# Kernel tuning notes

Hardware: AMD Instinct MI355X
Metric: run time of the kernel (lower is better)

## Reference

```python
import jax, jax.numpy as jnp
import numpy as np

HID = 16

def _mean_agg(feat, src, dst, n):
    # scatter-mean of source features into destination nodes (PyG aggr='mean')
    s = jax.ops.segment_sum(feat[src], dst, num_segments=n)
    deg = jax.ops.segment_sum(jnp.ones((src.shape[0], 1), feat.dtype), dst, num_segments=n)
    return s / jnp.maximum(deg, 1.0)


def setup_inputs() -> dict:
    key = jax.random.key(0)
    ks = jax.random.split(key, 12)
    N, E, F = 100000, 1600000, 64
    x = jax.random.normal(ks[0], (N, F), dtype=jnp.float32)
    edge_index = jax.random.randint(ks[1], (2, E), 0, N, dtype=jnp.int64)
    edge_weight = jnp.zeros((E,), dtype=jnp.int64)  # edge_type, relation 0 everywhere
    h_0 = jax.random.normal(ks[2], (N, HID), dtype=jnp.float32)
    c_0 = jax.random.normal(ks[3], (N, HID), dtype=jnp.float32)
    # stacked RGCNConv params for gates (i, f, c, o):
    #   Wx/Rx act on x (in=F), Wh/Rh act on h (in=HID); W=message weight, R=root weight
    sx = 1.0 / np.sqrt(F)
    sh = 1.0 / np.sqrt(HID)
    Wx = jax.random.normal(ks[4], (4, F, HID), dtype=jnp.float32) * sx
    Rx = jax.random.normal(ks[5], (4, F, HID), dtype=jnp.float32) * sx
    bx = jnp.zeros((4, HID), dtype=jnp.float32)
    Wh = jax.random.normal(ks[6], (4, HID, HID), dtype=jnp.float32) * sh
    Rh = jax.random.normal(ks[7], (4, HID, HID), dtype=jnp.float32) * sh
    bh = jnp.zeros((4, HID), dtype=jnp.float32)
    lin_w = jax.random.normal(ks[8], (HID, 1), dtype=jnp.float32) * sh
    lin_b = jnp.zeros((1,), dtype=jnp.float32)
    return {"x": x, "edge_index": edge_index, "edge_weight": edge_weight,
            "h_0": h_0, "c_0": c_0, "Wx": Wx, "Rx": Rx, "bx": bx,
            "Wh": Wh, "Rh": Rh, "bh": bh, "lin_w": lin_w, "lin_b": lin_b}


def reference(x, edge_index, edge_weight, h_0, c_0, Wx, Rx, bx, Wh, Rh, bh, lin_w, lin_b):
    # edge_weight is used by LRGCN as edge_type; with num_relations=1 it is all
    # zeros and every edge belongs to relation 0, so it drops out of the math.
    n = x.shape[0]
    src, dst = edge_index[0], edge_index[1]
    agg_x = _mean_agg(x, src, dst, n)    # [N, F]  shared across all 4 gates
    agg_h = _mean_agg(h_0, src, dst, n)  # [N, HID]
    # gate pre-activations: conv_x_g(x) + conv_h_g(h), g in {i,f,c,o}
    pre = (jnp.einsum('nd,gdo->gno', agg_x, Wx) + jnp.einsum('nd,gdo->gno', x, Rx)
           + bx[:, None, :]
           + jnp.einsum('nd,gdo->gno', agg_h, Wh) + jnp.einsum('nd,gdo->gno', h_0, Rh)
           + bh[:, None, :])  # [4, N, HID]
    i_g = jax.nn.sigmoid(pre[0])
    f_g = jax.nn.sigmoid(pre[1])
    t_g = jnp.tanh(pre[2])
    o_g = jax.nn.sigmoid(pre[3])
    c_new = f_g * c_0 + i_g * t_g
    h_new = o_g * jnp.tanh(c_new)
    out = jax.nn.relu(h_new) @ lin_w + lin_b  # [N, 1]
    return out, h_new, c_new
```

## Files before the change

kernel.cpp:

```cpp
#include <hip/hip_runtime.h>


#define F_IN 64
#define NHID 16
#define BSH  6
#define NPB  64
#define SEGW 512
#define PARTB (SEGW / 2)
#define EMAX 1280

__device__ __forceinline__ unsigned pack_bf16x2(float lo, float hi) {
    unsigned a = __float_as_uint(lo);
    unsigned b = __float_as_uint(hi);
    a = (a + 0x7fffu + ((a >> 16) & 1u)) >> 16;
    b = (b + 0x7fffu + ((b >> 16) & 1u)) >> 16;
    return a | (b << 16);
}
__device__ __forceinline__ float fast_sigmoid(float v) {
    return 1.f / (1.f + __expf(-v));
}
__device__ __forceinline__ float fast_tanh(float v) {
    return 1.f - 2.f / (1.f + __expf(2.f * v));
}
__device__ __forceinline__ void fma4(float4& a, float s, const float4& wv) {
    a.x += s * wv.x; a.y += s * wv.y; a.z += s * wv.z; a.w += s * wv.w;
}

__global__ __launch_bounds__(128) void fused_pp2(
        const int* __restrict__ ei, uint2* __restrict__ pairs,
        int* __restrict__ cnts, int E, int epw, int nbkt, int nbktp,
        const float* __restrict__ x, const float* __restrict__ h0,
        const float* __restrict__ Wx, const float* __restrict__ Wh,
        const float* __restrict__ Rx, const float* __restrict__ Rh,
        const float* __restrict__ bx, const float* __restrict__ bh,
        unsigned* __restrict__ mxb, unsigned* __restrict__ rootb,
        int n, int partBlocks) {
    extern __shared__ char smem[];
    int tid = threadIdx.x;

    if ((int)blockIdx.x < partBlocks) {
        int* cnt_s = (int*)smem;
        int wv = tid >> 6, lane = tid & 63;
        int seg = blockIdx.x * 2 + wv;
        int* cnt = cnt_s + wv * nbktp;

        for (int i = lane; i < nbktp; i += 64) cnt[i] = 0;
        __syncthreads();

        int beg = seg * epw;
        int end = beg + epw; if (end > E) end = E;

        for (int e = beg + lane; e < end; e += 64)
            atomicAdd(&cnt[((unsigned)ei[E + e]) >> BSH], 1);
        __syncthreads();

        int per = (nbkt + 63) >> 6;
        int s0 = lane * per;
        int s1 = s0 + per; if (s1 > nbkt) s1 = nbkt;
        if (s0 > nbkt) s0 = nbkt;
        int sum = 0;
        for (int i = s0; i < s1; ++i) sum += cnt[i];
        int inc = sum;
#pragma unroll
        for (int off = 1; off < 64; off <<= 1) {
            int v = __shfl_up(inc, off);
            if (lane >= off) inc += v;
        }
        int run = inc - sum;
        for (int i = s0; i < s1; ++i) { int c = cnt[i]; cnt[i] = run; run += c; }
        if (lane == 63) cnt[nbkt] = run;
        __syncthreads();

        for (int i = lane; i <= nbkt; i += 64)
            cnts[(size_t)seg * nbktp + i] = cnt[i];

        uint2* wreg = pairs + (size_t)seg * epw;
        for (int e = beg + lane; e < end; e += 64) {
            unsigned s = (unsigned)ei[e];
            unsigned d = (unsigned)ei[E + e];
            int pos = atomicAdd(&cnt[d >> BSH], 1);
            wreg[pos] = make_uint2(s, d);
        }
        return;
    }

    float* sx = (float*)smem;
    float* sh = sx + 32 * 68;
    int nodeBase = ((int)blockIdx.x - partBlocks) * 32;

#pragma unroll
    for (int i = 0; i < 4; ++i) {
        int idx = i * 128 + tid;
        int row = idx >> 4, c4 = idx & 15;
        int node = nodeBase + row;
        float4 v = make_float4(0.f, 0.f, 0.f, 0.f);
        if (node < n) v = ((const float4*)(x + (size_t)node * F_IN))[c4];
        *(float4*)(sx + row * 68 + c4 * 4) = v;
    }
    {
        int row = tid >> 2, c4 = tid & 3;
        int node = nodeBase + row;
        float4 v = make_float4(0.f, 0.f, 0.f, 0.f);
        if (node < n) v = ((const float4*)(h0 + (size_t)node * NHID))[c4];
        *(float4*)(sh + row * 20 + c4 * 4) = v;
    }
    __syncthreads();

    int grp = tid >> 4, q = tid & 15;
    int g = q >> 2, rr = q & 3;
    const float* wxp = Wx + g * (F_IN * NHID) + rr * 4;
    const float* rxp = Rx + g * (F_IN * NHID) + rr * 4;
    const float* whp = Wh + g * (NHID * NHID) + rr * 4;
    const float* rhp = Rh + g * (NHID * NHID) + rr * 4;
    const float* sx0 = sx + (grp * 4 + 0) * 68;
    const float* sx1 = sx + (grp * 4 + 1) * 68;
    const float* sx2 = sx + (grp * 4 + 2) * 68;
    const float* sx3 = sx + (grp * 4 + 3) * 68;
    const float* sh0 = sh + (grp * 4 + 0) * 20;
    const float* sh1 = sh + (grp * 4 + 1) * 20;
    const float* sh2 = sh + (grp * 4 + 2) * 20;
    const float* sh3 = sh + (grp * 4 + 3) * 20;

    float4 m0 = make_float4(0.f, 0.f, 0.f, 0.f), m1 = m0, m2 = m0, m3 = m0;
    float4 r0 = m0, r1 = m0, r2 = m0, r3 = m0;

    float4 w0 = *(const float4*)(wxp + 0 * NHID);
    float4 w1 = *(const float4*)(wxp + 1 * NHID);
    float4 w2 = *(const float4*)(wxp + 2 * NHID);
    float4 w3 = *(const float4*)(wxp + 3 * NHID);
    float4 v0 = *(const float4*)(rxp + 0 * NHID);
    float4 v1 = *(const float4*)(rxp + 1 * NHID);
    float4 v2 = *(const float4*)(rxp + 2 * NHID);
    float4 v3 = *(const float4*)(rxp + 3 * NHID);
#pragma unroll 1
    for (int k = 0; k < F_IN; k += 4) {
        float4 xa = *(const float4*)(sx0 + k);
        float4 xb = *(const float4*)(sx1 + k);
        float4 xc = *(const float4*)(sx2 + k);
        float4 xd = *(const float4*)(sx3 + k);
        int kn = (k + 4 < F_IN) ? k + 4 : 0;
        float4 t0 = *(const float4*)(wxp + (kn + 0) * NHID);
        float4 t1 = *(const float4*)(wxp + (kn + 1) * NHID);
        float4 t2 = *(const float4*)(wxp + (kn + 2) * NHID);
        float4 t3 = *(const float4*)(wxp + (kn + 3) * NHID);
        float4 u0 = *(const float4*)(rxp + (kn + 0) * NHID);
        float4 u1 = *(const float4*)(rxp + (kn + 1) * NHID);
        float4 u2 = *(const float4*)(rxp + (kn + 2) * NHID);
        float4 u3 = *(const float4*)(rxp + (kn + 3) * NHID);
        fma4(m0, xa.x, w0); fma4(m0, xa.y, w1); fma4(m0, xa.z, w2); fma4(m0, xa.w, w3);
        fma4(m1, xb.x, w0); fma4(m1, xb.y, w1); fma4(m1, xb.z, w2); fma4(m1, xb.w, w3);
        fma4(m2, xc.x, w0); fma4(m2, xc.y, w1); fma4(m2, xc.z, w2); fma4(m2, xc.w, w3);
        fma4(m3, xd.x, w0); fma4(m3, xd.y, w1); fma4(m3, xd.z, w2); fma4(m3, xd.w, w3);
        fma4(r0, xa.x, v0); fma4(r0, xa.y, v1); fma4(r0, xa.z, v2); fma4(r0, xa.w, v3);
        fma4(r1, xb.x, v0); fma4(r1, xb.y, v1); fma4(r1, xb.z, v2); fma4(r1, xb.w, v3);
        fma4(r2, xc.x, v0); fma4(r2, xc.y, v1); fma4(r2, xc.z, v2); fma4(r2, xc.w, v3);
        fma4(r3, xd.x, v0); fma4(r3, xd.y, v1); fma4(r3, xd.z, v2); fma4(r3, xd.w, v3);
        w0 = t0; w1 = t1; w2 = t2; w3 = t3;
        v0 = u0; v1 = u1; v2 = u2; v3 = u3;
    }
    w0 = *(const float4*)(whp + 0 * NHID);
    w1 = *(const float4*)(whp + 1 * NHID);
    w2 = *(const float4*)(whp + 2 * NHID);
    w3 = *(const float4*)(whp + 3 * NHID);
    v0 = *(const float4*)(rhp + 0 * NHID);
    v1 = *(const float4*)(rhp + 1 * NHID);
    v2 = *(const float4*)(rhp + 2 * NHID);
    v3 = *(const float4*)(rhp + 3 * NHID);
#pragma unroll 1
    for (int k = 0; k < NHID; k += 4) {
        float4 xa = *(const float4*)(sh0 + k);
        float4 xb = *(const float4*)(sh1 + k);
        float4 xc = *(const float4*)(sh2 + k);
        float4 xd = *(const float4*)(sh3 + k);
        int kn = (k + 4 < NHID) ? k + 4 : 0;
        float4 t0 = *(const float4*)(whp + (kn + 0) * NHID);
        float4 t1 = *(const float4*)(whp + (kn + 1) * NHID);
        float4 t2 = *(const float4*)(whp + (kn + 2) * NHID);
        float4 t3 = *(const float4*)(whp + (kn + 3) * NHID);
        float4 u0 = *(const float4*)(rhp + (kn + 0) * NHID);
        float4 u1 = *(const float4*)(rhp + (kn + 1) * NHID);
        float4 u2 = *(const float4*)(rhp + (kn + 2) * NHID);
        float4 u3 = *(const float4*)(rhp + (kn + 3) * NHID);
        fma4(m0, xa.x, w0); fma4(m0, xa.y, w1); fma4(m0, xa.z, w2); fma4(m0, xa.w, w3);
        fma4(m1, xb.x, w0); fma4(m1, xb.y, w1); fma4(m1, xb.z, w2); fma4(m1, xb.w, w3);
        fma4(m2, xc.x, w0); fma4(m2, xc.y, w1); fma4(m2, xc.z, w2); fma4(m2, xc.w, w3);
        fma4(m3, xd.x, w0); fma4(m3, xd.y, w1); fma4(m3, xd.z, w2); fma4(m3, xd.w, w3);
        fma4(r0, xa.x, v0); fma4(r0, xa.y, v1); fma4(r0, xa.z, v2); fma4(r0, xa.w, v3);
        fma4(r1, xb.x, v0); fma4(r1, xb.y, v1); fma4(r1, xb.z, v2); fma4(r1, xb.w, v3);
        fma4(r2, xc.x, v0); fma4(r2, xc.y, v1); fma4(r2, xc.z, v2); fma4(r2, xc.w, v3);
        fma4(r3, xd.x, v0); fma4(r3, xd.y, v1); fma4(r3, xd.z, v2); fma4(r3, xd.w, v3);
        w0 = t0; w1 = t1; w2 = t2; w3 = t3;
        v0 = u0; v1 = u1; v2 = u2; v3 = u3;
    }
    {
        float4 b1 = *(const float4*)(bx + q * 4);
        float4 b2 = *(const float4*)(bh + q * 4);
        float bxx = b1.x + b2.x, byy = b1.y + b2.y;
        float bzz = b1.z + b2.z, bww = b1.w + b2.w;
        r0.x += bxx; r0.y += byy; r0.z += bzz; r0.w += bww;
        r1.x += bxx; r1.y += byy; r1.z += bzz; r1.w += bww;
        r2.x += bxx; r2.y += byy; r2.z += bzz; r2.w += bww;
        r3.x += bxx; r3.y += byy; r3.z += bzz; r3.w += bww;
    }

    __syncthreads();
    *(float4*)(sx + (grp * 4 + 0) * 68 + q * 4) = m0;
    *(float4*)(sx + (grp * 4 + 1) * 68 + q * 4) = m1;
    *(float4*)(sx + (grp * 4 + 2) * 68 + q * 4) = m2;
    *(float4*)(sx + (grp * 4 + 3) * 68 + q * 4) = m3;
    __syncthreads();
#pragma unroll
    for (int i = 0; i < 4; ++i) {
        int node = nodeBase + grp * 4 + i;
        if (node < n) {
            const float* rowp = sx + (grp * 4 + i) * 68;
            float a0 = rowp[q], a1 = rowp[16 + q], a2 = rowp[32 + q], a3 = rowp[48 + q];
            ((uint2*)(mxb + (size_t)node * 32))[q] =
                make_uint2(pack_bf16x2(a0, a1), pack_bf16x2(a2, a3));
        }
    }
    if (rootb != nullptr) {
        __syncthreads();
        *(float4*)(sx + (grp * 4 + 0) * 68 + q * 4) = r0;
        *(float4*)(sx + (grp * 4 + 1) * 68 + q * 4) = r1;
        *(float4*)(sx + (grp * 4 + 2) * 68 + q * 4) = r2;
        *(float4*)(sx + (grp * 4 + 3) * 68 + q * 4) = r3;
        __syncthreads();
#pragma unroll
        for (int i = 0; i < 4; ++i) {
            int node = nodeBase + grp * 4 + i;
            if (node < n) {
                const float* rowp = sx + (grp * 4 + i) * 68;
                float a0 = rowp[q], a1 = rowp[16 + q], a2 = rowp[32 + q], a3 = rowp[48 + q];
                ((uint2*)(rootb + (size_t)node * 32))[q] =
                    make_uint2(pack_bf16x2(a0, a1), pack_bf16x2(a2, a3));
            }
        }
    }
}

__global__ __launch_bounds__(256) void hub_kernel(
        const float* __restrict__ c0, const float* __restrict__ lin_w,
        const float* __restrict__ lin_b,
        const unsigned* __restrict__ mxb, const unsigned* __restrict__ rootb,
        const uint2* __restrict__ pairs, const int* __restrict__ cnts,
        float* __restrict__ out, int n, int epw, int nbktp) {
    __shared__ int deg[NPB], rowptr[NPB], cursor[NPB];
    __shared__ unsigned stage[EMAX];
    __shared__ int csr[EMAX];
    __shared__ int scnt;
    int tid = threadIdx.x;

    int nb = gridDim.x;
    int qq = nb >> 3, rr2 = nb & 7;
    int xcd = blockIdx.x & 7, ix = blockIdx.x >> 3;
    int b = (xcd < rr2) ? xcd * (qq + 1) + ix
                        : rr2 * (qq + 1) + (xcd - rr2) * qq + ix;
    int nstart = b << BSH;

    if (tid < NPB) deg[tid] = 0;
    if (tid == 0) scnt = 0;
    __syncthreads();

    int seg0 = tid, seg1 = tid + 256;
    const int* cr0 = cnts + (size_t)seg0 * nbktp;
    const int* cr1 = cnts + (size_t)seg1 * nbktp;
    int o1a = cr0[b], o2a = cr0[b + 1];
    int o1b = cr1[b], o2b = cr1[b + 1];
    int tot = (o2a - o1a) + (o2b - o1b);
    int idx = 0;
    if (tot > 0) idx = atomicAdd(&scnt, tot);
    {
        const uint2* p = pairs + (size_t)seg0 * epw;
        for (int i = o1a; i < o2a; ++i, ++idx) {
            uint2 pr = p[i];
            if (idx < EMAX) {
                int dl = (int)pr.y - nstart;
                stage[idx] = pr.x | ((unsigned)dl << 26);
                atomicAdd(&deg[dl], 1);
            }
        }
        p = pairs + (size_t)seg1 * epw;
        for (int i = o1b; i < o2b; ++i, ++idx) {
            uint2 pr = p[i];
            if (idx < EMAX) {
                int dl = (int)pr.y - nstart;
                stage[idx] = pr.x | ((unsigned)dl << 26);
                atomicAdd(&deg[dl], 1);
            }
        }
    }
    __syncthreads();

    if (tid < 64) {
        int lane = tid;
        int v = deg[lane];
        int inc = v;
#pragma unroll
        for (int off = 1; off < 64; off <<= 1) {
            int t = __shfl_up(inc, off);
            if (lane >= off) inc += t;
        }
        rowptr[lane] = inc - v;
        cursor[lane] = inc - v;
    }
    __syncthreads();

    int sc = scnt < EMAX ? scnt : EMAX;
    for (int i = tid; i < sc; i += 256) {
        unsigned v = stage[i];
        int dl = v >> 26;
        int pos = atomicAdd(&cursor[dl], 1);
        csr[pos] = (int)(v & 0x03FFFFFFu);
    }
    __syncthreads();

    int grp = tid >> 4, q = tid & 15;
    for (int ln = grp; ln < NPB; ln += 16) {
        int node = nstart + ln;
        if (node >= n) continue;
        int cnt = deg[ln];
        const int* row = &csr[rowptr[ln]];

        float ax = 0.f, ay = 0.f, az = 0.f, aw = 0.f;
        int base = 0;
        for (; base + 16 <= cnt; base += 16) {
            int eid = row[base + q];
#pragma unroll
            for (int k = 0; k < 16; ++k) {
                int s = __shfl(eid, k, 16);
                uint2 v = *((const uint2*)(mxb + (size_t)s * 32) + q);
                ax += __uint_as_float(v.x << 16);
                ay += __uint_as_float(v.x & 0xffff0000u);
                az += __uint_as_float(v.y << 16);
                aw += __uint_as_float(v.y & 0xffff0000u);
            }
        }
        int m = cnt - base;
        if (m > 0) {
            int eid = (q < m) ? row[base + q] : 0;
            for (int k = 0; k < m; ++k) {
                int s = __shfl(eid, k, 16);
                uint2 v = *((const uint2*)(mxb + (size_t)s * 32) + q);
                ax += __uint_as_float(v.x << 16);
                ay += __uint_as_float(v.x & 0xffff0000u);
                az += __uint_as_float(v.y << 16);
                aw += __uint_as_float(v.y & 0xffff0000u);
            }
        }

        uint2 rv = *((const uint2*)(rootb + (size_t)node * 32) + q);
        float inv = 1.f / fmaxf((float)cnt, 1.f);
        float px = ax * inv + __uint_as_float(rv.x << 16);
        float py = ay * inv + __uint_as_float(rv.x & 0xffff0000u);
        float pz = az * inv + __uint_as_float(rv.y << 16);
        float pw = aw * inv + __uint_as_float(rv.y & 0xffff0000u);

        float ig = fast_sigmoid(px);
        float fg = fast_sigmoid(py);
        float tg = fast_tanh(pz);
        float og = fast_sigmoid(pw);

        float cn = fg * c0[(size_t)node * NHID + q] + ig * tg;
        float hn = og * fast_tanh(cn);

        out[(size_t)n + (size_t)node * NHID + q] = hn;
        out[(size_t)n + (size_t)n * NHID + (size_t)node * NHID + q] = cn;

        float p = fmaxf(hn, 0.f) * lin_w[q];
#pragma unroll
        for (int off = 8; off; off >>= 1) p += __shfl_xor(p, off, 16);
        if (q == 0) out[node] = p + lin_b[0];
    }
}

__global__ void zero_int_kernel(int4* __restrict__ p, int n4) {
    int i = blockIdx.x * blockDim.x + threadIdx.x;
    if (i < n4) p[i] = make_int4(0, 0, 0, 0);
}
__global__ void scatter_direct_kernel(const int* __restrict__ ei,
                                      int* __restrict__ cursor,
                                      int* __restrict__ csrp, int E, int cap) {
    int e = blockIdx.x * blockDim.x + threadIdx.x;
    if (e < E) {
        int d = ei[E + e];
        int pos = atomicAdd(&cursor[d], 1);
        if (pos < cap) csrp[(size_t)d * cap + pos] = ei[e];
    }
}
__global__ __launch_bounds__(256) void gfinal_inl(
        const float* __restrict__ x, const float* __restrict__ h0,
        const float* __restrict__ c0,
        const float* __restrict__ Rx, const float* __restrict__ Rh,
        const float* __restrict__ bx, const float* __restrict__ bh,
        const float* __restrict__ lin_w, const float* __restrict__ lin_b,
        const unsigned* __restrict__ mxb, const int* __restrict__ csrp,
        const int* __restrict__ cursor,
        float* __restrict__ out, int n, int cap) {
    __shared__ float sm[16 * 68];
    int idx = blockIdx.x * 256 + threadIdx.x;
    int node = idx >> 4, q = idx & 15;
    int nl = threadIdx.x >> 4;
    bool valid = node < n;

    int cnt = 0;
    if (valid) cnt = cursor[node];
    int mt = cnt < cap ? cnt : cap;
    const int* row = csrp + (size_t)node * cap;

    float ax = 0.f, ay = 0.f, az = 0.f, aw = 0.f;
    int base = 0;
    for (; base + 16 <= mt; base += 16) {
        int eid = row[base + q];
#pragma unroll
        for (int k = 0; k < 16; ++k) {
            int s = __shfl(eid, k, 16);
            uint2 v = *((const uint2*)(mxb + (size_t)s * 32) + q);
            ax += __uint_as_float(v.x << 16);
            ay += __uint_as_float(v.x & 0xffff0000u);
            az += __uint_as_float(v.y << 16);
            aw += __uint_as_float(v.y & 0xffff0000u);
        }
    }
    int mrem = mt - base;
    if (mrem > 0) {
        int eid = (q < mrem) ? row[base + q] : 0;
        for (int k = 0; k < mrem; ++k) {
            int s = __shfl(eid, k, 16);
            uint2 v = *((const uint2*)(mxb + (size_t)s * 32) + q);
            ax += __uint_as_float(v.x << 16);
            ay += __uint_as_float(v.x & 0xffff0000u);
            az += __uint_as_float(v.y << 16);
            aw += __uint_as_float(v.y & 0xffff0000u);
        }
    }

    float4 r = make_float4(0.f, 0.f, 0.f, 0.f);
    if (valid) {
        int g = q >> 2, rr = q & 3;
        const float* xr = x + (size_t)node * F_IN;
        const float* hr = h0 + (size_t)node * NHID;
        const float* rx = Rx + g * (F_IN * NHID) + rr * 4;
        const float* rh = Rh + g * (NHID * NHID) + rr * 4;
#pragma unroll 8
        for (int k = 0; k < F_IN; ++k) fma4(r, xr[k], *(const float4*)(rx + k * NHID));
#pragma unroll
        for (int k = 0; k < NHID; ++k) fma4(r, hr[k], *(const float4*)(rh + k * NHID));
        float4 b1 = *(const float4*)(bx + q * 4);
        float4 b2 = *(const float4*)(bh + q * 4);
        r.x += b1.x + b2.x; r.y += b1.y + b2.y;
        r.z += b1.z + b2.z; r.w += b1.w + b2.w;
    }
    *(float4*)(sm + nl * 68 + q * 4) = r;
    __syncthreads();

    if (valid) {
        const float* rowp = sm + nl * 68;
        float inv = 1.f / fmaxf((float)cnt, 1.f);
        float px = ax * inv + rowp[q];
        float py = ay * inv + rowp[16 + q];
        float pz = az * inv + rowp[32 + q];
        float pw = aw * inv + rowp[48 + q];
        float ig = fast_sigmoid(px);
        float fg = fast_sigmoid(py);
        float tg = fast_tanh(pz);
        float og = fast_sigmoid(pw);
        float cn = fg * c0[(size_t)node * NHID + q] + ig * tg;
        float hn = og * fast_tanh(cn);
        out[(size_t)n + (size_t)node * NHID + q] = hn;
        out[(size_t)n + (size_t)n * NHID + (size_t)node * NHID + q] = cn;
        float p = fmaxf(hn, 0.f) * lin_w[q];
#pragma unroll
        for (int off = 8; off; off >>= 1) p += __shfl_xor(p, off, 16);
        if (q == 0) out[node] = p + lin_b[0];
    }
}

extern "C" void kernel_launch(void* const* d_in, const int* in_sizes, int n_in,
                              void* d_out, int out_size, void* d_ws, size_t ws_size,
                              hipStream_t stream) {
    const float* x     = (const float*)d_in[0];
    const int*   ei    = (const int*)d_in[1];
    const float* h0    = (const float*)d_in[3];
    const float* c0    = (const float*)d_in[4];
    const float* Wx    = (const float*)d_in[5];
    const float* Rx    = (const float*)d_in[6];
    const float* bx    = (const float*)d_in[7];
    const float* Wh    = (const float*)d_in[8];
    const float* Rh    = (const float*)d_in[9];
    const float* bh    = (const float*)d_in[10];
    const float* lin_w = (const float*)d_in[11];
    const float* lin_b = (const float*)d_in[12];

    const int N = in_sizes[3] / NHID;
    const int E = in_sizes[1] / 2;
    const int NBKT  = (N + NPB - 1) >> BSH;
    const int nbktp = ((NBKT + 1) + 15) & ~15;
    const int epw   = ((E + SEGW - 1) / SEGW + 7) & ~7;

    const size_t mxb_u   = (size_t)N * 32;
    const size_t root_u  = (size_t)N * 32;
    const size_t pairs_u = 2ull * SEGW * epw;
    const size_t cnts_u  = (size_t)SEGW * nbktp;
    const size_t need = (mxb_u + root_u + pairs_u + cnts_u) * 4;

    unsigned* wsu = (unsigned*)d_ws;
    float* out = (float*)d_out;
    const int projBlocks = (N + 31) / 32;

    size_t ldsPart = (size_t)2 * nbktp * sizeof(int);
    size_t ldsProj = (32 * 68 + 32 * 20) * sizeof(float);
    size_t ldsFused = ldsPart > ldsProj ? ldsPart : ldsProj;

    if (ws_size >= need) {
        unsigned* mxb   = wsu;
        unsigned* rootb = mxb + mxb_u;
        uint2*    pairs = (uint2*)(rootb + root_u);
        int*      cnts  = (int*)(pairs + (size_t)SEGW * epw);

        fused_pp2<<<PARTB + projBlocks, 128, (int)ldsFused, stream>>>(
            ei, pairs, cnts, E, epw, NBKT, nbktp,
            x, h0, Wx, Wh, Rx, Rh, bx, bh, mxb, rootb, N, PARTB);
        hub_kernel<<<NBKT, 256, 0, stream>>>(
            c0, lin_w, lin_b, mxb, rootb, pairs, cnts, out, N, epw, nbktp);
    } else {
        const int cap = 32;
        const int P = (N + 3) & ~3;
        unsigned* mxb   = wsu;
        int*      cursor= (int*)(mxb + mxb_u);
        int*      csrp  = cursor + P;

        zero_int_kernel<<<(P / 4 + 255) / 256, 256, 0, stream>>>((int4*)cursor, P / 4);
        fused_pp2<<<projBlocks, 128, (int)ldsProj, stream>>>(
            ei, nullptr, nullptr, E, epw, NBKT, nbktp,
            x, h0, Wx, Wh, Rx, Rh, bx, bh, mxb, nullptr, N, 0);
        scatter_direct_kernel<<<(E + 255) / 256, 256, 0, stream>>>(
            ei, cursor, csrp, E, cap);
        gfinal_inl<<<(N * 16 + 255) / 256, 256, 0, stream>>>(
            x, h0, c0, Rx, Rh, bx, bh, lin_w, lin_b, mxb, csrp, cursor,
            out, N, cap);
    }
}
```

Before: 140.3 us.

## Stage gate weights in LDS and double block size of fused partition/projection kernel

Block size of fused_pp2 doubles to 256 threads. Partition blocks now cover four segments each and projection blocks cover 64 nodes each. All Wx/Rx/Wh/Rh weights are copied into padded LDS once per block, and the matmul loops read them from LDS instead of prefetching from global memory through registers. The goal is to cut repeated global/L1 weight traffic and register pressure from software prefetch, at the cost of roughly 64KB of LDS per block, which may limit occupancy. The code not shown after the projection matmul must still handle the 64-node tile correctly.

```diff
diff --git a/kernel.cpp b/kernel.cpp
--- a/kernel.cpp
+++ b/kernel.cpp
@@ -6,8 +6,16 @@
 #define BSH  6
 #define NPB  64
 #define SEGW 512
-#define PARTB (SEGW / 2)
+#define PARTB (SEGW / 4)
 #define EMAX 1280
+
+#define LWX 0
+#define LRX 4128
+#define LWH 8256
+#define LRH 9312
+#define LSX 10368
+#define LSH 14720
+#define LDSF 16000
 
 __device__ __forceinline__ unsigned pack_bf16x2(float lo, float hi) {
     unsigned a = __float_as_uint(lo);
@@ -26,7 +34,7 @@
     a.x += s * wv.x; a.y += s * wv.y; a.z += s * wv.z; a.w += s * wv.w;
 }
 
-__global__ __launch_bounds__(128) void fused_pp2(
+__global__ __launch_bounds__(256) void fused_pp2(
         const int* __restrict__ ei, uint2* __restrict__ pairs,
         int* __restrict__ cnts, int E, int epw, int nbkt, int nbktp,
         const float* __restrict__ x, const float* __restrict__ h0,
@@ -35,13 +43,13 @@
         const float* __restrict__ bx, const float* __restrict__ bh,
         unsigned* __restrict__ mxb, unsigned* __restrict__ rootb,
         int n, int partBlocks) {
-    extern __shared__ char smem[];
+    extern __shared__ float smem[];
     int tid = threadIdx.x;
 
     if ((int)blockIdx.x < partBlocks) {
         int* cnt_s = (int*)smem;
         int wv = tid >> 6, lane = tid & 63;
-        int seg = blockIdx.x * 2 + wv;
+        int seg = blockIdx.x * 4 + wv;
         int* cnt = cnt_s + wv * nbktp;
 
         for (int i = lane; i < nbktp; i += 64) cnt[i] = 0;
@@ -84,13 +92,32 @@
         return;
     }
 
-    float* sx = (float*)smem;
-    float* sh = sx + 32 * 68;
-    int nodeBase = ((int)blockIdx.x - partBlocks) * 32;
+    float* lwx = smem + LWX;
+    float* lrx = smem + LRX;
+    float* lwh = smem + LWH;
+    float* lrh = smem + LRH;
+    float* sx  = smem + LSX;
+    float* sh  = smem + LSH;
+    int nodeBase = ((int)blockIdx.x - partBlocks) * 64;
 
 #pragma unroll
     for (int i = 0; i < 4; ++i) {
-        int idx = i * 128 + tid;
+        int idx = i * 256 + tid;
+        int gg = idx >> 8;
+        int off = (idx & 255) * 4;
+        *(float4*)(lwx + gg * 1032 + off) = ((const float4*)Wx)[idx];
+        *(float4*)(lrx + gg * 1032 + off) = ((const float4*)Rx)[idx];
+    }
+    {
+        int idx = tid;
+        int gg = idx >> 6;
+        int off = (idx & 63) * 4;
+        *(float4*)(lwh + gg * 264 + off) = ((const float4*)Wh)[idx];
+        *(float4*)(lrh + gg * 264 + off) = ((const float4*)Rh)[idx];
+    }
+#pragma unroll
+    for (int i = 0; i < 4; ++i) {
+        int idx = i * 256 + tid;
         int row = idx >> 4, c4 = idx & 15;
         int node = nodeBase + row;
         float4 v = make_float4(0.f, 0.f, 0.f, 0.f);
@@ -108,10 +135,10 @@
 
     int grp = tid >> 4, q = tid & 15;
     int g = q >> 2, rr = q & 3;
-    const float* wxp = Wx + g * (F_IN * NHID) + rr * 4;
-    const float* rxp = Rx + g * (F_IN * NHID) + rr * 4;
-    const float* whp = Wh + g * (NHID * NHID) + rr * 4;
-    const float* rhp = Rh + g * (NHID * NHID) + rr * 4;
+    const float* wxp = lwx + g * 1032 + rr * 4;
+    const float* rxp = lrx + g * 1032 + rr * 4;
+    const float* whp = lwh + g * 264 + rr * 4;
+    const float* rhp = lrh + g * 264 + rr * 4;
     const float* sx0 = sx + (grp * 4 + 0) * 68;
     const float* sx1 = sx + (grp * 4 + 1) * 68;
     const float* sx2 = sx + (grp * 4 + 2) * 68;
@@ -124,29 +151,20 @@
     float4 m0 = make_float4(0.f, 0.f, 0.f, 0.f), m1 = m0, m2 = m0, m3 = m0;
     float4 r0 = m0, r1 = m0, r2 = m0, r3 = m0;
 
-    float4 w0 = *(const float4*)(wxp + 0 * NHID);
-    float4 w1 = *(const float4*)(wxp + 1 * NHID);
-    float4 w2 = *(const float4*)(wxp + 2 * NHID);
-    float4 w3 = *(const float4*)(wxp + 3 * NHID);
-    float4 v0 = *(const float4*)(rxp + 0 * NHID);
-    float4 v1 = *(const float4*)(rxp + 1 * NHID);
-    float4 v2 = *(const float4*)(rxp + 2 * NHID);
-    float4 v3 = *(const float4*)(rxp + 3 * NHID);
 #pragma unroll 1
     for (int k = 0; k < F_IN; k += 4) {
         float4 xa = *(const float4*)(sx0 + k);
         float4 xb = *(const float4*)(sx1 + k);
         float4 xc = *(const float4*)(sx2 + k);
         float4 xd = *(const float4*)(sx3 + k);
-        int kn = (k + 4 < F_IN) ? k + 4 : 0;
-        float4 t0 = *(const float4*)(wxp + (kn + 0) * NHID);
-        float4 t1 = *(const float4*)(wxp + (kn + 1) * NHID);
-        float4 t2 = *(const float4*)(wxp + (kn + 2) * NHID);
-        float4 t3 = *(const float4*)(wxp + (kn + 3) * NHID);
-        float4 u0 = *(const float4*)(rxp + (kn + 0) * NHID);
-        float4 u1 = *(const float4*)(rxp + (kn + 1) * NHID);
-        float4 u2 = *(const float4*)(rxp + (kn + 2) * NHID);
-        float4 u3 = *(const float4*)(rxp + (kn + 3) * NHID);
+        float4 w0 = *(const float4*)(wxp + (k + 0) * NHID);
+        float4 w1 = *(const float4*)(wxp + (k + 1) * NHID);
+        float4 w2 = *(const float4*)(wxp + (k + 2) * NHID);
+        float4 w3 = *(const float4*)(wxp + (k + 3) * NHID);
+        float4 v0 = *(const float4*)(rxp + (k + 0) * NHID);
+        float4 v1 = *(const float4*)(rxp + (k + 1) * NHID);
+        float4 v2 = *(const float4*)(rxp + (k + 2) * NHID);
+        float4 v3 = *(const float4*)(rxp + (k + 3) * NHID);
         fma4(m0, xa.x, w0); fma4(m0, xa.y, w1); fma4(m0, xa.z, w2); fma4(m0, xa.w, w3);
         fma4(m1, xb.x, w0); fma4(m1, xb.y, w1); fma4(m1, xb.z, w2); fma4(m1, xb.w, w3);
         fma4(m2, xc.x, w0); fma4(m2, xc.y, w1); fma4(m2, xc.z, w2); fma4(m2, xc.w, w3);
@@ -155,32 +173,21 @@
         fma4(r1, xb.x, v0); fma4(r1, xb.y, v1); fma4(r1, xb.z, v2); fma4(r1, xb.w, v3);
         fma4(r2, xc.x, v0); fma4(r2, xc.y, v1); fma4(r2, xc.z, v2); fma4(r2, xc.w, v3);
         fma4(r3, xd.x, v0); fma4(r3, xd.y, v1); fma4(r3, xd.z, v2); fma4(r3, xd.w, v3);
-        w0 = t0; w1 = t1; w2 = t2; w3 = t3;
-        v0 = u0; v1 = u1; v2 = u2; v3 = u3;
-    }
-    w0 = *(const float4*)(whp + 0 * NHID);
-    w1 = *(const float4*)(whp + 1 * NHID);
-    w2 = *(const float4*)(whp + 2 * NHID);
-    w3 = *(const float4*)(whp + 3 * NHID);
-    v0 = *(const float4*)(rhp + 0 * NHID);
-    v1 = *(const float4*)(rhp + 1 * NHID);
-    v2 = *(const float4*)(rhp + 2 * NHID);
-    v3 = *(const float4*)(rhp + 3 * NHID);
+    }
 #pragma unroll 1
     for (int k = 0; k < NHID; k += 4) {
         float4 xa = *(const float4*)(sh0 + k);
         float4 xb = *(const float4*)(sh1 + k);
         float4 xc = *(const float4*)(sh2 + k);
         float4 xd = *(const float4*)(sh3 + k);
-        int kn = (k + 4 < NHID) ? k + 4 : 0;
-        float4 t0 = *(const float4*)(whp + (kn + 0) * NHID);
-        float4 t1 = *(const float4*)(whp + (kn + 1) * NHID);
-        float4 t2 = *(const float4*)(whp + (kn + 2) * NHID);
-        float4 t3 = *(const float4*)(whp + (kn + 3) * NHID);
-        float4 u0 = *(const float4*)(rhp + (kn + 0) * NHID);
-        float4 u1 = *(const float4*)(rhp + (kn + 1) * NHID);
-        float4 u2 = *(const float4*)(rhp + (kn + 2) * NHID);
-        float4 u3 = *(const float4*)(rhp + (kn + 3) * NHID);
+        float4 w0 = *(const float4*)(whp + (k + 0) * NHID);
+        float4 w1 = *(const float4*)(whp + (k + 1) * NHID);
+        float4 w2 = *(const float4*)(whp + (k + 2) * NHID);
+        float4 w3 = *(const float4*)(whp + (k + 3) * NHID);
+        float4 v0 = *(const float4*)(rhp + (k + 0) * NHID);
+        float4 v1 = *(const float4*)(rhp + (k + 1) * NHID);
+        float4 v2 = *(const float4*)(rhp + (k + 2) * NHID);
+        float4 v3 = *(const float4*)(rhp + (k + 3) * NHID);
         fma4(m0, xa.x, w0); fma4(m0, xa.y, w1); fma4(m0, xa.z, w2); fma4(m0, xa.w, w3);
         fma4(m1, xb.x, w0); fma4(m1, xb.y, w1); fma4(m1, xb.z, w2); fma4(m1, xb.w, w3);
         fma4(m2, xc.x, w0); fma4(m2, xc.y, w1); fma4(m2, xc.z, w2); fma4(m2, xc.w, w3);
@@ -189,8 +196,6 @@
         fma4(r1, xb.x, v0); fma4(r1, xb.y, v1); fma4(r1, xb.z, v2); fma4(r1, xb.w, v3);
         fma4(r2, xc.x, v0); fma4(r2, xc.y, v1); fma4(r2, xc.z, v2); fma4(r2, xc.w, v3);
         fma4(r3, xd.x, v0); fma4(r3, xd.y, v1); fma4(r3, xd.z, v2); fma4(r3, xd.w, v3);
-        w0 = t0; w1 = t1; w2 = t2; w3 = t3;
-        v0 = u0; v1 = u1; v2 = u2; v3 = u3;
     }
     {
         float4 b1 = *(const float4*)(bx + q * 4);
@@ -506,10 +511,10 @@
 
     unsigned* wsu = (unsigned*)d_ws;
     float* out = (float*)d_out;
-    const int projBlocks = (N + 31) / 32;
-
-    size_t ldsPart = (size_t)2 * nbktp * sizeof(int);
-    size_t ldsProj = (32 * 68 + 32 * 20) * sizeof(float);
+    const int projBlocks = (N + 63) / 64;
+
+    size_t ldsPart = (size_t)4 * nbktp * sizeof(int);
+    size_t ldsProj = (size_t)LDSF * sizeof(float);
     size_t ldsFused = ldsPart > ldsProj ? ldsPart : ldsProj;
 
     if (ws_size >= need) {
@@ -518,7 +523,7 @@
         uint2*    pairs = (uint2*)(rootb + root_u);
         int*      cnts  = (int*)(pairs + (size_t)SEGW * epw);
 
-        fused_pp2<<<PARTB + projBlocks, 128, (int)ldsFused, stream>>>(
+        fused_pp2<<<PARTB + projBlocks, 256, (int)ldsFused, stream>>>(
             ei, pairs, cnts, E, epw, NBKT, nbktp,
             x, h0, Wx, Wh, Rx, Rh, bx, bh, mxb, rootb, N, PARTB);
         hub_kernel<<<NBKT, 256, 0, stream>>>(
@@ -531,7 +536,7 @@
         int*      csrp  = cursor + P;
 
         zero_int_kernel<<<(P / 4 + 255) / 256, 256, 0, stream>>>((int4*)cursor, P / 4);
-        fused_pp2<<<projBlocks, 128, (int)ldsProj, stream>>>(
+        fused_pp2<<<projBlocks, 256, (int)ldsProj, stream>>>(
             ei, nullptr, nullptr, E, epw, NBKT, nbktp,
             x, h0, Wx, Wh, Rx, Rh, bx, bh, mxb, nullptr, N, 0);
         scatter_direct_kernel<<<(E + 255) / 256, 256, 0, stream>>>(
```

Measured after the change: 117.7 us (median of 2 runs). -16.1%, faster.
